# Optimization experiments

Measured on AMD Instinct MI355X. Metric: run time of the kernel, lower is better.

The kernel has to match this reference:

```python
import jax, jax.numpy as jnp
import numpy as np

N = 100000   # nodes
E = 6400000  # edges (avg degree 64)
F = 512      # num_features
C = 16       # num_classes

def _glorot(key, shape):
    fan_in, fan_out = shape
    lim = (6.0 / (fan_in + fan_out)) ** 0.5
    return jax.random.uniform(key, shape, jnp.float32, -lim, lim)

def setup_inputs() -> dict:
    key = jax.random.key(0)
    ks = jax.random.split(key, 8)
    x = jax.random.normal(ks[0], (N, F), jnp.float32)
    edge_index = jax.random.randint(ks[1], (2, E), 0, N, dtype=jnp.int64)
    return {
        "x": x,
        "edge_index": edge_index,
        "W1": _glorot(ks[2], (F, 16)), "b1": jnp.zeros((16,), jnp.float32),
        "W2": _glorot(ks[3], (16, 32)), "b2": jnp.zeros((32,), jnp.float32),
        "W3": _glorot(ks[4], (32, C)),  "b3": jnp.zeros((C,), jnp.float32),
        "Wc": _glorot(ks[5], (C, C)),   "bc": jnp.zeros((C,), jnp.float32),
    }

def _gcn_conv(x, row, col, norm, W, b):
    # PyG GCNConv: transform, then normalized sum-aggregation, then bias
    h = x @ W                                   # [N, out]
    msg = h[row] * norm[:, None]                # gather + scale, [E+N, out]
    agg = jax.ops.segment_sum(msg, col, num_segments=N)
    return agg + b

def reference(x, edge_index, W1, b1, W2, b2, W3, b3, Wc, bc):
    n = x.shape[0]
    loops = jnp.arange(n, dtype=edge_index.dtype)
    row = jnp.concatenate([edge_index[0], loops])  # source
    col = jnp.concatenate([edge_index[1], loops])  # target
    # symmetric normalization D^{-1/2} A_hat D^{-1/2}
    deg = jax.ops.segment_sum(jnp.ones_like(col, dtype=x.dtype), col, num_segments=n)
    dis = jnp.where(deg > 0, jax.lax.rsqrt(deg), 0.0)
    norm = dis[row] * dis[col]                     # [E+N]
    h = jax.nn.relu(_gcn_conv(x, row, col, norm, W1, b1))
    h = jax.nn.relu(_gcn_conv(h, row, col, norm, W2, b2))
    h = jax.nn.relu(_gcn_conv(h, row, col, norm, W3, b3))
    out = h @ Wc + bc
    return (out, h)
```

## Files before the change

kernel.cpp:

```cpp
#include <hip/hip_runtime.h>
#include <hip/hip_bf16.h>
#include <hip/hip_fp16.h>
#include <stdint.h>


__device__ __forceinline__ int blockScanExclusive256(int v, int* wsum) {
  int lane = threadIdx.x & 63;
  int wid  = threadIdx.x >> 6;
  int inc = v;
#pragma unroll
  for (int d = 1; d < 64; d <<= 1) {
    int y = __shfl_up(inc, d, 64);
    if (lane >= d) inc += y;
  }
  if (lane == 63) wsum[wid] = inc;
  __syncthreads();
  if (threadIdx.x == 0) {
    int s = 0;
#pragma unroll
    for (int w = 0; w < 4; ++w) { int t = wsum[w]; wsum[w] = s; s += t; }
  }
  __syncthreads();
  return inc - v + wsum[wid];
}

__device__ __forceinline__ int blockScanExclusive512(int v, int* wsum) {
  int lane = threadIdx.x & 63;
  int wid  = threadIdx.x >> 6;
  int inc = v;
#pragma unroll
  for (int d = 1; d < 64; d <<= 1) {
    int y = __shfl_up(inc, d, 64);
    if (lane >= d) inc += y;
  }
  if (lane == 63) wsum[wid] = inc;
  __syncthreads();
  if (threadIdx.x == 0) {
    int s = 0;
#pragma unroll
    for (int w = 0; w < 8; ++w) { int t = wsum[w]; wsum[w] = s; s += t; }
  }
  __syncthreads();
  return inc - v + wsum[wid];
}

__global__ __launch_bounds__(256) void k_bhist(const int* __restrict__ ecol,
                                               int* __restrict__ cntmat,
                                               int e, int chunk, int nb) {
  __shared__ int h[256];
  h[threadIdx.x] = 0;
  __syncthreads();
  int g = blockIdx.x, G = gridDim.x;
  int s0 = g * chunk;
  int s1 = min(e, s0 + chunk);
  int i = s0 + threadIdx.x;
  for (; i + 768 < s1; i += 1024) {
    int c0 = ecol[i], c1 = ecol[i + 256], c2 = ecol[i + 512], c3 = ecol[i + 768];
    atomicAdd(&h[c0 >> 9], 1);
    atomicAdd(&h[c1 >> 9], 1);
    atomicAdd(&h[c2 >> 9], 1);
    atomicAdd(&h[c3 >> 9], 1);
  }
  for (; i < s1; i += 256) atomicAdd(&h[ecol[i] >> 9], 1);
  __syncthreads();
  for (int b = threadIdx.x; b < nb; b += 256) cntmat[b * G + g] = h[b];
}

__global__ __launch_bounds__(256) void k_colscan(int* __restrict__ cntmat,
                                                 int* __restrict__ colsum, int G) {
  __shared__ int wsum[4];
  __shared__ int carry_s;
  int b = blockIdx.x;
  if (threadIdx.x == 0) carry_s = 0;
  __syncthreads();
  for (int base = 0; base < G; base += 256) {
    int i = base + threadIdx.x;
    int v = (i < G) ? cntmat[b * G + i] : 0;
    int ex = blockScanExclusive256(v, wsum);
    int c = carry_s;
    __syncthreads();
    if (i < G) cntmat[b * G + i] = ex + c;
    if (threadIdx.x == 255) carry_s = c + ex + v;
    __syncthreads();
  }
  if (threadIdx.x == 0) colsum[b] = carry_s;
}

__global__ __launch_bounds__(256) void k_bscan(const int* __restrict__ colsum,
                                               int* __restrict__ bbase,
                                               int nb, int etot) {
  __shared__ int wsum[4];
  __shared__ int carry_s;
  if (threadIdx.x == 0) carry_s = 0;
  __syncthreads();
  for (int base = 0; base < nb; base += 256) {
    int i = base + threadIdx.x;
    int v = (i < nb) ? colsum[i] : 0;
    int ex = blockScanExclusive256(v, wsum);
    int c = carry_s;
    __syncthreads();
    if (i < nb) bbase[i] = ex + c;
    if (threadIdx.x == 255) carry_s = c + ex + v;
    __syncthreads();
  }
  if (threadIdx.x == 0) bbase[nb] = etot;
}

__global__ __launch_bounds__(256) void k_scat_xf(
    const int* __restrict__ erow, const int* __restrict__ ecol,
    const int* __restrict__ cntmat, const int* __restrict__ bbase,
    unsigned* __restrict__ sorted, int e, int chunk, int nb,
    const float* __restrict__ x, const float* __restrict__ W,
    __half* __restrict__ t1raw, int n) {
  __shared__ int base[256];
  int g = blockIdx.x, G = gridDim.x;
  for (int b = threadIdx.x; b < nb; b += 256)
    base[b] = bbase[b] + cntmat[b * G + g];
  __syncthreads();
  int s0 = g * chunk;
  int s1 = min(e, s0 + chunk);
  {
    int i = s0 + threadIdx.x;
    for (; i + 768 < s1; i += 1024) {
      int c0 = ecol[i],       c1 = ecol[i + 256], c2 = ecol[i + 512], c3 = ecol[i + 768];
      int r0 = erow[i],       r1 = erow[i + 256], r2 = erow[i + 512], r3 = erow[i + 768];
      int p0 = atomicAdd(&base[c0 >> 9], 1);
      int p1 = atomicAdd(&base[c1 >> 9], 1);
      int p2 = atomicAdd(&base[c2 >> 9], 1);
      int p3 = atomicAdd(&base[c3 >> 9], 1);
      sorted[p0] = ((unsigned)r0 << 9) | (unsigned)(c0 & 511);
      sorted[p1] = ((unsigned)r1 << 9) | (unsigned)(c1 & 511);
      sorted[p2] = ((unsigned)r2 << 9) | (unsigned)(c2 & 511);
      sorted[p3] = ((unsigned)r3 << 9) | (unsigned)(c3 & 511);
    }
    for (; i < s1; i += 256) {
      int c = ecol[i];
      int p = atomicAdd(&base[c >> 9], 1);
      sorted[p] = ((unsigned)erow[i] << 9) | (unsigned)(c & 511);
    }
  }

  int L = threadIdx.x & 63;
  int wid = blockIdx.x * 4 + (threadIdx.x >> 6);
  int nw = gridDim.x * 4;

  float w[8][16];
  const float4* W4 = reinterpret_cast<const float4*>(W);
#pragma unroll
  for (int i = 0; i < 4; ++i) {
#pragma unroll
    for (int c4 = 0; c4 < 4; ++c4) {
      float4 va = W4[(4 * L + i) * 4 + c4];
      w[i][c4 * 4 + 0] = va.x; w[i][c4 * 4 + 1] = va.y;
      w[i][c4 * 4 + 2] = va.z; w[i][c4 * 4 + 3] = va.w;
      float4 vb = W4[(256 + 4 * L + i) * 4 + c4];
      w[4 + i][c4 * 4 + 0] = vb.x; w[4 + i][c4 * 4 + 1] = vb.y;
      w[4 + i][c4 * 4 + 2] = vb.z; w[4 + i][c4 * 4 + 3] = vb.w;
    }
  }
  int col = ((L & 1) << 3) | ((L & 2) << 1) | ((L & 4) >> 1) | ((L & 8) >> 3);

  for (int r = wid; r < n; r += nw) {
    const float4* xr = reinterpret_cast<const float4*>(x + (size_t)r * 512);
    float4 v0 = xr[L];
    float4 v1 = xr[64 + L];
    float acc[16];
#pragma unroll
    for (int c = 0; c < 16; ++c) {
      float a = v0.x * w[0][c];
      a = fmaf(v0.y, w[1][c], a);
      a = fmaf(v0.z, w[2][c], a);
      a = fmaf(v0.w, w[3][c], a);
      a = fmaf(v1.x, w[4][c], a);
      a = fmaf(v1.y, w[5][c], a);
      a = fmaf(v1.z, w[6][c], a);
      a = fmaf(v1.w, w[7][c], a);
      acc[c] = a;
    }
#pragma unroll
    for (int j = 0; j < 8; ++j) {
      float send = (L & 1) ? acc[j] : acc[j + 8];
      float recv = __shfl_xor(send, 1, 64);
      acc[j] = ((L & 1) ? acc[j + 8] : acc[j]) + recv;
    }
#pragma unroll
    for (int j = 0; j < 4; ++j) {
      float send = (L & 2) ? acc[j] : acc[j + 4];
      float recv = __shfl_xor(send, 2, 64);
      acc[j] = ((L & 2) ? acc[j + 4] : acc[j]) + recv;
    }
#pragma unroll
    for (int j = 0; j < 2; ++j) {
      float send = (L & 4) ? acc[j] : acc[j + 2];
      float recv = __shfl_xor(send, 4, 64);
      acc[j] = ((L & 4) ? acc[j + 2] : acc[j]) + recv;
    }
    {
      float send = (L & 8) ? acc[0] : acc[1];
      float recv = __shfl_xor(send, 8, 64);
      acc[0] = ((L & 8) ? acc[1] : acc[0]) + recv;
    }
    float s = acc[0];
    s += __shfl_xor(s, 16, 64);
    s += __shfl_xor(s, 32, 64);
    if (L < 16) t1raw[r * 16 + col] = __float2half(s);
  }
}

__global__ __launch_bounds__(512) void k_pass2(const unsigned* __restrict__ sorted,
                                               const int* __restrict__ bbase,
                                               float* __restrict__ dis,
                                               int* __restrict__ rowptr,
                                               __half* __restrict__ t1,
                                               int* __restrict__ csr,
                                               int n, int etot) {
  __shared__ int hist[512];
  __shared__ int cur[512];
  __shared__ int wsum[8];
  int b = blockIdx.x;
  hist[threadIdx.x] = 0;
  __syncthreads();
  int s0 = bbase[b], s1 = bbase[b + 1];
  for (int i = s0 + threadIdx.x; i < s1; i += 512)
    atomicAdd(&hist[sorted[i] & 511], 1);
  __syncthreads();
  int j = threadIdx.x;
  int node = (b << 9) + j;
  int deg = hist[j];
  int ex = blockScanExclusive512(deg, wsum);
  float dv = rsqrtf((float)(deg + 1));
  cur[j] = s0 + ex;
  if (node < n) {
    dis[node] = dv;
    rowptr[node] = s0 + ex;
    __half2* t2 = reinterpret_cast<__half2*>(t1 + ((size_t)node << 4));
#pragma unroll
    for (int q = 0; q < 8; ++q) {
      float2 fv = __half22float2(t2[q]);
      fv.x *= dv; fv.y *= dv;
      t2[q] = __float22half2_rn(fv);
    }
  }
  if (b == 0 && threadIdx.x == 0) rowptr[n] = etot;
  __syncthreads();
  for (int i = s0 + threadIdx.x; i < s1; i += 512) {
    unsigned v = sorted[i];
    int pos = atomicAdd(&cur[v & 511], 1);
    csr[pos] = (int)(v >> 9);
  }
}

__device__ __forceinline__ float gather16(const __half* __restrict__ hs,
                                          const int* __restrict__ rowptr,
                                          const int* __restrict__ csr,
                                          int node, int f) {
  float acc0 = __half2float(hs[(node << 4) + f]);
  int e0 = rowptr[node], e1 = rowptr[node + 1];
  int e = e0;
  float acc1 = 0.f, acc2 = 0.f, acc3 = 0.f;
  for (; e + 16 <= e1; e += 16) {
    int r0  = csr[e + 0],  r1  = csr[e + 1],  r2  = csr[e + 2],  r3  = csr[e + 3];
    int r4  = csr[e + 4],  r5  = csr[e + 5],  r6  = csr[e + 6],  r7  = csr[e + 7];
    int r8  = csr[e + 8],  r9  = csr[e + 9],  r10 = csr[e + 10], r11 = csr[e + 11];
    int r12 = csr[e + 12], r13 = csr[e + 13], r14 = csr[e + 14], r15 = csr[e + 15];
    __half v0  = hs[(r0  << 4) + f], v1  = hs[(r1  << 4) + f];
    __half v2  = hs[(r2  << 4) + f], v3  = hs[(r3  << 4) + f];
    __half v4  = hs[(r4  << 4) + f], v5  = hs[(r5  << 4) + f];
    __half v6  = hs[(r6  << 4) + f], v7  = hs[(r7  << 4) + f];
    __half v8  = hs[(r8  << 4) + f], v9  = hs[(r9  << 4) + f];
    __half v10 = hs[(r10 << 4) + f], v11 = hs[(r11 << 4) + f];
    __half v12 = hs[(r12 << 4) + f], v13 = hs[(r13 << 4) + f];
    __half v14 = hs[(r14 << 4) + f], v15 = hs[(r15 << 4) + f];
    acc0 += (__half2float(v0)  + __half2float(v1))  + (__half2float(v2)  + __half2float(v3));
    acc1 += (__half2float(v4)  + __half2float(v5))  + (__half2float(v6)  + __half2float(v7));
    acc2 += (__half2float(v8)  + __half2float(v9))  + (__half2float(v10) + __half2float(v11));
    acc3 += (__half2float(v12) + __half2float(v13)) + (__half2float(v14) + __half2float(v15));
  }
  for (; e + 4 <= e1; e += 4) {
    int r0 = csr[e + 0], r1 = csr[e + 1], r2 = csr[e + 2], r3 = csr[e + 3];
    float v0 = __half2float(hs[(r0 << 4) + f]), v1 = __half2float(hs[(r1 << 4) + f]);
    float v2 = __half2float(hs[(r2 << 4) + f]), v3 = __half2float(hs[(r3 << 4) + f]);
    acc0 += (v0 + v1) + (v2 + v3);
  }
  for (; e < e1; ++e) acc0 += __half2float(hs[(csr[e] << 4) + f]);
  return (acc0 + acc1) + (acc2 + acc3);
}

__global__ __launch_bounds__(256) void k_agg_rb(
    const __half* __restrict__ hs, const int* __restrict__ rowptr,
    const int* __restrict__ csr, const float* __restrict__ dis,
    const float* __restrict__ b, __half* __restrict__ out, int n) {
  int node = blockIdx.x * 16 + threadIdx.x / 16;
  int f = threadIdx.x % 16;
  if (node >= n) return;
  float acc = gather16(hs, rowptr, csr, node, f);
  float d = dis[node];
  float t = fmaxf(fmaf(d, acc, b[f]), 0.f);
  out[(node << 4) + f] = __float2half(t * d);
}

__global__ __launch_bounds__(256) void k_agg_mid(
    const __half* __restrict__ hs, const int* __restrict__ rowptr,
    const int* __restrict__ csr, const float* __restrict__ dis,
    const float* __restrict__ W2, const float* __restrict__ b2,
    const float* __restrict__ W3, __half* __restrict__ out, int n) {
  __shared__ float w2s[512];
  __shared__ float w3s[512];
  __shared__ float b2s[32];
  for (int i = threadIdx.x; i < 512; i += 256) { w2s[i] = W2[i]; w3s[i] = W3[i]; }
  if (threadIdx.x < 32) b2s[threadIdx.x] = b2[threadIdx.x];
  __syncthreads();
  int node = blockIdx.x * 16 + threadIdx.x / 16;
  int f = threadIdx.x % 16;
  if (node >= n) return;
  float acc = gather16(hs, rowptr, csr, node, f);
  float d = dis[node];
  float v = d * acc;
  int base = threadIdx.x & 48;
  float a0 = b2s[f], a1 = b2s[f + 16];
#pragma unroll
  for (int k = 0; k < 16; ++k) {
    float vk = __shfl(v, base + k, 64);
    a0 = fmaf(vk, w2s[k * 32 + f], a0);
    a1 = fmaf(vk, w2s[k * 32 + 16 + f], a1);
  }
  a0 = fmaxf(a0, 0.f);
  a1 = fmaxf(a1, 0.f);
  float t = 0.f;
#pragma unroll
  for (int c = 0; c < 16; ++c) {
    float h0 = __shfl(a0, base + c, 64);
    float h1 = __shfl(a1, base + c, 64);
    t = fmaf(h0, w3s[c * 16 + f], t);
    t = fmaf(h1, w3s[(c + 16) * 16 + f], t);
  }
  out[(node << 4) + f] = __float2half(t * d);
}

__global__ __launch_bounds__(256) void k_agg_out(
    const __half* __restrict__ hs, const int* __restrict__ rowptr,
    const int* __restrict__ csr, const float* __restrict__ dis,
    const float* __restrict__ b3, const float* __restrict__ Wc,
    const float* __restrict__ bc, float* __restrict__ outh,
    float* __restrict__ outc, int n) {
  __shared__ float wcs[256];
  __shared__ float b3s[16];
  __shared__ float bcs[16];
  if (threadIdx.x < 256) wcs[threadIdx.x] = Wc[threadIdx.x];
  if (threadIdx.x < 16) { b3s[threadIdx.x] = b3[threadIdx.x]; bcs[threadIdx.x] = bc[threadIdx.x]; }
  __syncthreads();
  int node = blockIdx.x * 16 + threadIdx.x / 16;
  int f = threadIdx.x % 16;
  if (node >= n) return;
  float acc = gather16(hs, rowptr, csr, node, f);
  float d = dis[node];
  float h = fmaxf(fmaf(d, acc, b3s[f]), 0.f);
  outh[(node << 4) + f] = h;
  int base = threadIdx.x & 48;
  float o = bcs[f];
#pragma unroll
  for (int k = 0; k < 16; ++k) {
    float hk = __shfl(h, base + k, 64);
    o = fmaf(hk, wcs[k * 16 + f], o);
  }
  outc[(node << 4) + f] = o;
}

extern "C" void kernel_launch(void* const* d_in, const int* in_sizes, int n_in,
                              void* d_out, int out_size, void* d_ws, size_t ws_size,
                              hipStream_t stream) {
  (void)n_in; (void)out_size;
  const float* x  = (const float*)d_in[0];
  const int*   ei = (const int*)d_in[1];
  const float* W1 = (const float*)d_in[2];
  const float* b1 = (const float*)d_in[3];
  const float* W2 = (const float*)d_in[4];
  const float* b2 = (const float*)d_in[5];
  const float* W3 = (const float*)d_in[6];
  const float* b3 = (const float*)d_in[7];
  const float* Wc = (const float*)d_in[8];
  const float* bc = (const float*)d_in[9];

  const int F = 512;
  int N = in_sizes[0] / F;
  int E = in_sizes[1] / 2;
  const int* erow = ei;
  const int* ecol = ei + E;
  int NB = (N + 511) >> 9;
  const int G = 4096;
  int chunk = (E + G - 1) / G;

  auto align = [](size_t v) { return (v + 255) & ~(size_t)255; };
  char* p = (char*)d_ws;
  int*   cntmat = (int*)p;   p += align((size_t)NB * G * 4);
  int*   colsum = (int*)p;   p += align(256 * 4);
  int*   bbase  = (int*)p;   p += align(257 * 4);
  float* dis    = (float*)p; p += align((size_t)N * 4);
  int*   rowptr = (int*)p;   p += align(((size_t)N + 1) * 4);
  int*   csr    = (int*)p;   p += align((size_t)E * 4);
  unsigned* sorted = (unsigned*)p; p += align((size_t)E * 4);
  __half* bufA = (__half*)p; p += align((size_t)N * 16 * 2);
  __half* bufB = (__half*)p; p += align((size_t)N * 16 * 2);
  if ((size_t)(p - (char*)d_ws) > ws_size) return;

  float* outc = (float*)d_out;
  float* outh = (float*)d_out + (size_t)N * 16;

  k_bhist<<<G, 256, 0, stream>>>(ecol, cntmat, E, chunk, NB);
  k_colscan<<<NB, 256, 0, stream>>>(cntmat, colsum, G);
  k_bscan<<<1, 256, 0, stream>>>(colsum, bbase, NB, E);
  k_scat_xf<<<G, 256, 0, stream>>>(erow, ecol, cntmat, bbase, sorted, E, chunk,
                                   NB, x, W1, bufA, N);
  k_pass2<<<NB, 512, 0, stream>>>(sorted, bbase, dis, rowptr, bufA, csr, N, E);

  k_agg_rb<<<(N + 15) / 16, 256, 0, stream>>>(bufA, rowptr, csr, dis, b1, bufB, N);
  k_agg_mid<<<(N + 15) / 16, 256, 0, stream>>>(bufB, rowptr, csr, dis, W2, b2, W3, bufA, N);
  k_agg_out<<<(N + 15) / 16, 256, 0, stream>>>(bufA, rowptr, csr, dis, b3, Wc, bc, outh, outc, N);
}
```

Measured before the change: 361.7 us.

## Split scatter and feature-transform into separate block groups, shrink histogram grid

The fused scatter/transform kernel now assigns the first 512 blocks only to bucket-scattering edges and the remaining 1536 blocks only to the x@W1 transform, where before every block did both phases in sequence. The histogram grid drops from 4096 to 512 chunks, and the count matrix is transposed to chunk-major so the histogram writes are coalesced. The aim is to shrink the count matrix and the column-scan work, and to let the scatter and the dense transform run concurrently on different CUs. In exchange, each scatter chunk is longer, so shared-memory atomic contention per block goes up.

```diff
diff --git a/kernel.cpp b/kernel.cpp
--- a/kernel.cpp
+++ b/kernel.cpp
@@ -50,7 +50,7 @@
   __shared__ int h[256];
   h[threadIdx.x] = 0;
   __syncthreads();
-  int g = blockIdx.x, G = gridDim.x;
+  int g = blockIdx.x;
   int s0 = g * chunk;
   int s1 = min(e, s0 + chunk);
   int i = s0 + threadIdx.x;
@@ -63,11 +63,12 @@
   }
   for (; i < s1; i += 256) atomicAdd(&h[ecol[i] >> 9], 1);
   __syncthreads();
-  for (int b = threadIdx.x; b < nb; b += 256) cntmat[b * G + g] = h[b];
+  for (int b = threadIdx.x; b < nb; b += 256) cntmat[g * nb + b] = h[b];
 }
 
 __global__ __launch_bounds__(256) void k_colscan(int* __restrict__ cntmat,
-                                                 int* __restrict__ colsum, int G) {
+                                                 int* __restrict__ colsum,
+                                                 int G, int nb) {
   __shared__ int wsum[4];
   __shared__ int carry_s;
   int b = blockIdx.x;
@@ -75,11 +76,11 @@
   __syncthreads();
   for (int base = 0; base < G; base += 256) {
     int i = base + threadIdx.x;
-    int v = (i < G) ? cntmat[b * G + i] : 0;
+    int v = (i < G) ? cntmat[i * nb + b] : 0;
     int ex = blockScanExclusive256(v, wsum);
     int c = carry_s;
     __syncthreads();
-    if (i < G) cntmat[b * G + i] = ex + c;
+    if (i < G) cntmat[i * nb + b] = ex + c;
     if (threadIdx.x == 255) carry_s = c + ex + v;
     __syncthreads();
   }
@@ -109,17 +110,17 @@
 __global__ __launch_bounds__(256) void k_scat_xf(
     const int* __restrict__ erow, const int* __restrict__ ecol,
     const int* __restrict__ cntmat, const int* __restrict__ bbase,
-    unsigned* __restrict__ sorted, int e, int chunk, int nb,
+    unsigned* __restrict__ sorted, int e, int chunk, int nb, int gs,
     const float* __restrict__ x, const float* __restrict__ W,
     __half* __restrict__ t1raw, int n) {
-  __shared__ int base[256];
-  int g = blockIdx.x, G = gridDim.x;
-  for (int b = threadIdx.x; b < nb; b += 256)
-    base[b] = bbase[b] + cntmat[b * G + g];
-  __syncthreads();
-  int s0 = g * chunk;
-  int s1 = min(e, s0 + chunk);
-  {
+  if ((int)blockIdx.x < gs) {
+    __shared__ int base[256];
+    int g = blockIdx.x;
+    for (int b = threadIdx.x; b < nb; b += 256)
+      base[b] = bbase[b] + cntmat[g * nb + b];
+    __syncthreads();
+    int s0 = g * chunk;
+    int s1 = min(e, s0 + chunk);
     int i = s0 + threadIdx.x;
     for (; i + 768 < s1; i += 1024) {
       int c0 = ecol[i],       c1 = ecol[i + 256], c2 = ecol[i + 512], c3 = ecol[i + 768];
@@ -138,11 +139,12 @@
       int p = atomicAdd(&base[c >> 9], 1);
       sorted[p] = ((unsigned)erow[i] << 9) | (unsigned)(c & 511);
     }
+    return;
   }
 
   int L = threadIdx.x & 63;
-  int wid = blockIdx.x * 4 + (threadIdx.x >> 6);
-  int nw = gridDim.x * 4;
+  int wid = (blockIdx.x - gs) * 4 + (threadIdx.x >> 6);
+  int nw = (gridDim.x - gs) * 4;
 
   float w[8][16];
   const float4* W4 = reinterpret_cast<const float4*>(W);
@@ -387,12 +389,13 @@
   const int* erow = ei;
   const int* ecol = ei + E;
   int NB = (N + 511) >> 9;
-  const int G = 4096;
-  int chunk = (E + G - 1) / G;
+  const int GS = 512;
+  const int GT = 1536;
+  int chunk = (E + GS - 1) / GS;
 
   auto align = [](size_t v) { return (v + 255) & ~(size_t)255; };
   char* p = (char*)d_ws;
-  int*   cntmat = (int*)p;   p += align((size_t)NB * G * 4);
+  int*   cntmat = (int*)p;   p += align((size_t)GS * NB * 4);
   int*   colsum = (int*)p;   p += align(256 * 4);
   int*   bbase  = (int*)p;   p += align(257 * 4);
   float* dis    = (float*)p; p += align((size_t)N * 4);
@@ -406,11 +409,11 @@
   float* outc = (float*)d_out;
   float* outh = (float*)d_out + (size_t)N * 16;
 
-  k_bhist<<<G, 256, 0, stream>>>(ecol, cntmat, E, chunk, NB);
-  k_colscan<<<NB, 256, 0, stream>>>(cntmat, colsum, G);
+  k_bhist<<<GS, 256, 0, stream>>>(ecol, cntmat, E, chunk, NB);
+  k_colscan<<<NB, 256, 0, stream>>>(cntmat, colsum, GS, NB);
   k_bscan<<<1, 256, 0, stream>>>(colsum, bbase, NB, E);
-  k_scat_xf<<<G, 256, 0, stream>>>(erow, ecol, cntmat, bbase, sorted, E, chunk,
-                                   NB, x, W1, bufA, N);
+  k_scat_xf<<<GS + GT, 256, 0, stream>>>(erow, ecol, cntmat, bbase, sorted, E,
+                                         chunk, NB, GS, x, W1, bufA, N);
   k_pass2<<<NB, 512, 0, stream>>>(sorted, bbase, dis, rowptr, bufA, csr, N, E);
 
   k_agg_rb<<<(N + 15) / 16, 256, 0, stream>>>(bufA, rowptr, csr, dis, b1, bufB, N);
```

Result: faster. 318.5 us (-11.9%).
